# Optimization experiments

Hardware: AMD Instinct MI355X
Metric: run time of the kernel (lower is better)

Reference implementation:

```python
import jax, jax.numpy as jnp
import numpy as np

N, E = 50000, 800000
D_IN, D_HID, D_OUT = 128, 128, 64
BN_EPS = 1e-5
GEN_EPS = 1e-7


def _lin_init(k, fan_in, shape):
    lim = 1.0 / np.sqrt(fan_in)
    return jax.random.uniform(k, shape, minval=-lim, maxval=lim, dtype=jnp.float32)


def setup_inputs() -> dict:
    key = jax.random.key(0)
    ks = jax.random.split(key, 12)
    x = jax.random.normal(ks[0], (N, D_IN), dtype=jnp.float32)
    edge_index = jax.random.randint(ks[1], (2, E), 0, N, dtype=jnp.int64)
    return {
        "x": x,
        # GCNConv 0 and 1 (Glorot-ish uniform init like PyG Linear)
        "W0": _lin_init(ks[2], D_IN, (D_IN, D_HID)), "b0": jnp.zeros((D_HID,), jnp.float32),
        "g0": jnp.ones((D_HID,), jnp.float32), "beta0": jnp.zeros((D_HID,), jnp.float32),
        "W1": _lin_init(ks[3], D_HID, (D_HID, D_HID)), "b1": jnp.zeros((D_HID,), jnp.float32),
        "g1": jnp.ones((D_HID,), jnp.float32), "beta1": jnp.zeros((D_HID,), jnp.float32),
        # GENConv MLP: [D_HID] -> [2*D_HID] (BN+ReLU) -> [D_OUT]
        "Wg1": _lin_init(ks[4], D_HID, (D_HID, 2 * D_HID)), "bg1": jnp.zeros((2 * D_HID,), jnp.float32),
        "gg": jnp.ones((2 * D_HID,), jnp.float32), "betag": jnp.zeros((2 * D_HID,), jnp.float32),
        "Wg2": _lin_init(ks[5], 2 * D_HID, (2 * D_HID, D_OUT)), "bg2": jnp.zeros((D_OUT,), jnp.float32),
        "edge_index": edge_index,
    }


def _bn(h, gamma, beta):
    # BatchNorm1d, training-mode batch statistics (biased variance)
    mu = jnp.mean(h, axis=0)
    var = jnp.mean(jnp.square(h - mu), axis=0)
    return (h - mu) * jax.lax.rsqrt(var + BN_EPS) * gamma + beta


def _gcn_conv(x, W, b, src, dst, n):
    # GCNConv: D^-1/2 (A + I) D^-1/2 (x W) + b
    loop = jnp.arange(n, dtype=src.dtype)
    s = jnp.concatenate([src, loop])
    d = jnp.concatenate([dst, loop])
    deg = jax.ops.segment_sum(jnp.ones_like(s, dtype=x.dtype), d, num_segments=n)
    dinv = jax.lax.rsqrt(deg)  # deg >= 1 due to self-loops
    norm = dinv[s] * dinv[d]   # [E+N]
    h = x @ W                  # [N, D]
    agg = jax.ops.segment_sum(norm[:, None] * h[s], d, num_segments=n)
    return agg + b


def _gen_conv(x, W1, b1, g, beta, W2, b2, src, dst, n):
    # GENConv (defaults): msg = relu(x_j) + eps; per-channel softmax aggregation
    # (t=1); residual add of x_dst; then MLP [D, 2D (BN+ReLU), D_out].
    msg = jax.nn.relu(x[src]) + GEN_EPS            # [E, D]
    m = jax.ops.segment_max(msg, dst, num_segments=n)
    m = jnp.where(jnp.isfinite(m), m, 0.0)         # guard zero in-degree nodes
    ex = jnp.exp(msg - m[dst])                     # [E, D]
    denom = jax.ops.segment_sum(ex, dst, num_segments=n)
    num = jax.ops.segment_sum(ex * msg, dst, num_segments=n)
    agg = num / jnp.maximum(denom, 1e-16)          # [N, D]
    out = agg + x                                  # residual
    h = jax.nn.relu(_bn(out @ W1 + b1, g, beta))
    return h @ W2 + b2


def reference(x, W0, b0, g0, beta0, W1, b1, g1, beta1,
              Wg1, bg1, gg, betag, Wg2, bg2, edge_index):
    src, dst = edge_index[0], edge_index[1]
    n = x.shape[0]
    # layer 0: GCNConv -> BN -> ReLU (dropout is identity in eval)
    h = _gcn_conv(x, W0, b0, src, dst, n)
    h = jax.nn.relu(_bn(h, g0, beta0))
    # layer 1
    h = _gcn_conv(h, W1, b1, src, dst, n)
    h = jax.nn.relu(_bn(h, g1, beta1))
    # final GENConv + log-softmax over classes
    h = _gen_conv(h, Wg1, bg1, gg, betag, Wg2, bg2, src, dst, n)
    return jax.nn.log_softmax(h, axis=-1)
```

## Files before the change

kernel.cpp:

```cpp
#include <hip/hip_runtime.h>
#include <hip/hip_bf16.h>

#define DIN 128
#define DHID 128
#define DCLS 64
#define BN_EPS 1e-5f
#define GEN_EPS 1e-7f

typedef __attribute__((ext_vector_type(8))) short short8;
typedef __attribute__((ext_vector_type(4))) float f32x4;

static __device__ __forceinline__ float bf2f(unsigned short u) {
    union { float f; unsigned int i; } x; x.i = ((unsigned int)u) << 16; return x.f;
}
static __device__ __forceinline__ unsigned short f2bf(float f) {
    union { float f; unsigned int i; } x; x.f = f;
    unsigned int r = x.i + 0x7fffu + ((x.i >> 16) & 1u);
    return (unsigned short)(r >> 16);
}
static __device__ __forceinline__ float bflo(unsigned int u) {
    union { float f; unsigned int i; } x; x.i = u << 16; return x.f;
}
static __device__ __forceinline__ float bfhi(unsigned int u) {
    union { float f; unsigned int i; } x; x.i = u & 0xffff0000u; return x.f;
}
static __device__ __forceinline__ unsigned int packbf(float lo, float hi) {
    return ((unsigned int)f2bf(hi) << 16) | f2bf(lo);
}

__global__ void k_hist(const int* __restrict__ dst, int* __restrict__ counts, int E) {
    int e = blockIdx.x * 256 + threadIdx.x;
    if (e < E) atomicAdd(&counts[dst[e]], 1);
}

__global__ __launch_bounds__(256) void k_scan1(const int* __restrict__ counts,
        int* __restrict__ roff, int* __restrict__ bsum, int N) {
    __shared__ int ls[256];
    int t = threadIdx.x;
    int base = blockIdx.x * 1024 + t * 4;
    int c0 = 0, c1 = 0, c2 = 0, c3 = 0;
    if (base + 3 < N) {
        int4 v = *(const int4*)(counts + base);
        c0 = v.x; c1 = v.y; c2 = v.z; c3 = v.w;
    } else {
        if (base + 0 < N) c0 = counts[base + 0];
        if (base + 1 < N) c1 = counts[base + 1];
        if (base + 2 < N) c2 = counts[base + 2];
        if (base + 3 < N) c3 = counts[base + 3];
    }
    ls[t] = c0 + c1 + c2 + c3;
    __syncthreads();
    for (int off = 1; off < 256; off <<= 1) {
        int v = (t >= off) ? ls[t - off] : 0;
        __syncthreads();
        ls[t] += v;
        __syncthreads();
    }
    int r = (t == 0) ? 0 : ls[t - 1];
    if (base + 0 < N) { roff[base + 0] = r; r += c0; }
    if (base + 1 < N) { roff[base + 1] = r; r += c1; }
    if (base + 2 < N) { roff[base + 2] = r; r += c2; }
    if (base + 3 < N) { roff[base + 3] = r; }
    if (t == 255) bsum[blockIdx.x] = ls[255];
}

__global__ __launch_bounds__(1024) void k_scan2(int* __restrict__ bsum, int nblk) {
    __shared__ int ls[1024];
    int t = threadIdx.x;
    ls[t] = (t < nblk) ? bsum[t] : 0;
    __syncthreads();
    for (int off = 1; off < 1024; off <<= 1) {
        int v = (t >= off) ? ls[t - off] : 0;
        __syncthreads();
        ls[t] += v;
        __syncthreads();
    }
    if (t < nblk) bsum[t] = (t == 0) ? 0 : ls[t - 1];
}

__global__ void k_scan3(const int* __restrict__ counts, const int* __restrict__ bsum,
        int* __restrict__ roff, int* __restrict__ cursor, float* __restrict__ dinv,
        int N, int E) {
    int i = blockIdx.x * 256 + threadIdx.x;
    if (i < N) {
        int r = roff[i] + bsum[i >> 10];
        roff[i] = r; cursor[i] = r;
        dinv[i] = rsqrtf((float)(counts[i] + 1));
    }
    if (i == 0) roff[N] = E;
}

__global__ void k_fill(const int* __restrict__ src, const int* __restrict__ dst,
        int* __restrict__ cursor, int* __restrict__ srcs, int E) {
    int e = blockIdx.x * 256 + threadIdx.x;
    if (e < E) {
        int d = dst[e];
        int p = atomicAdd(&cursor[d], 1);
        srcs[p] = src[e];
    }
}

__global__ void k_wt(const float* __restrict__ W, unsigned short* __restrict__ Wt, int K, int Dout) {
    int i = blockIdx.x * 256 + threadIdx.x;
    if (i >= K * Dout) return;
    int n = i / K, k = i - n * K;
    Wt[i] = f2bf(W[(size_t)k * Dout + n]);
}

template<int K, bool ABF16, bool OBF16>
__global__ __launch_bounds__(256) void k_gemm(const void* __restrict__ Av,
        const unsigned short* __restrict__ Wt, const float* __restrict__ bias,
        const float* __restrict__ scale, const float* __restrict__ shift,
        const float* __restrict__ rowscale,
        void* __restrict__ Cv, int nrows, int Dout) {
    constexpr int KP = K + 8;
    __shared__ unsigned short sA[64 * KP];
    __shared__ unsigned short sW[64 * KP];
    const int tid = threadIdx.x;
    const int row0 = blockIdx.x * 64, col0 = blockIdx.y * 64;

#pragma unroll
    for (int it = 0; it < (64 * K) / (256 * 4); ++it) {
        int idx = (it * 256 + tid) * 4;
        int r = idx / K, c = idx % K;
        int gr = row0 + r;
        float v0 = 0.f, v1 = 0.f, v2 = 0.f, v3 = 0.f;
        if (gr < nrows) {
            if (ABF16) {
                ushort4 u = *(const ushort4*)((const unsigned short*)Av + (size_t)gr * K + c);
                v0 = bf2f(u.x); v1 = bf2f(u.y); v2 = bf2f(u.z); v3 = bf2f(u.w);
            } else {
                float4 f = *(const float4*)((const float*)Av + (size_t)gr * K + c);
                v0 = f.x; v1 = f.y; v2 = f.z; v3 = f.w;
            }
            if (scale) {
                v0 = fmaxf(v0 * scale[c + 0] + shift[c + 0], 0.f);
                v1 = fmaxf(v1 * scale[c + 1] + shift[c + 1], 0.f);
                v2 = fmaxf(v2 * scale[c + 2] + shift[c + 2], 0.f);
                v3 = fmaxf(v3 * scale[c + 3] + shift[c + 3], 0.f);
            }
        }
        ushort4 o; o.x = f2bf(v0); o.y = f2bf(v1); o.z = f2bf(v2); o.w = f2bf(v3);
        *(ushort4*)(&sA[r * KP + c]) = o;
    }
#pragma unroll
    for (int it = 0; it < (64 * K) / (256 * 8); ++it) {
        int idx = (it * 256 + tid) * 8;
        int r = idx / K, c = idx % K;
        uint4 u = *(const uint4*)(Wt + (size_t)(col0 + r) * K + c);
        *(uint4*)(&sW[r * KP + c]) = u;
    }
    __syncthreads();

    const int w = tid >> 6, lane = tid & 63;
    const int wr = (w >> 1) * 32, wc = (w & 1) * 32;
    const int lr = lane & 15, kg = (lane >> 4) * 8;
    f32x4 acc[2][2] = {};
#pragma unroll
    for (int kk = 0; kk < K; kk += 32) {
        short8 af[2], bfr[2];
#pragma unroll
        for (int mi = 0; mi < 2; mi++)
            af[mi] = *(const short8*)(&sA[(wr + mi * 16 + lr) * KP + kk + kg]);
#pragma unroll
        for (int ni = 0; ni < 2; ni++)
            bfr[ni] = *(const short8*)(&sW[(wc + ni * 16 + lr) * KP + kk + kg]);
#pragma unroll
        for (int mi = 0; mi < 2; mi++)
#pragma unroll
            for (int ni = 0; ni < 2; ni++)
                acc[mi][ni] = __builtin_amdgcn_mfma_f32_16x16x32_bf16(af[mi], bfr[ni], acc[mi][ni], 0, 0, 0);
    }
#pragma unroll
    for (int mi = 0; mi < 2; mi++) {
#pragma unroll
        for (int ni = 0; ni < 2; ni++) {
            int r = wr + mi * 16 + (lane >> 4) * 4;
            int cgl = col0 + wc + ni * 16 + (lane & 15);
            float bv = bias ? bias[cgl] : 0.f;
#pragma unroll
            for (int j = 0; j < 4; j++) {
                int gr = row0 + r + j;
                if (gr < nrows) {
                    float val = acc[mi][ni][j] + bv;
                    if (rowscale) val *= rowscale[gr];
                    if (OBF16) ((unsigned short*)Cv)[(size_t)gr * Dout + cgl] = f2bf(val);
                    else       ((float*)Cv)[(size_t)gr * Dout + cgl] = val;
                }
            }
        }
    }
}

__global__ __launch_bounds__(256) void k_gcn_agg(const unsigned short* __restrict__ p,
        const int* __restrict__ roff, const int* __restrict__ srcs,
        const float* __restrict__ dinv, const float* __restrict__ b,
        unsigned short* __restrict__ out,
        float* __restrict__ gsum, float* __restrict__ gsq, int N) {
    int nw = (gridDim.x * 256) >> 6;
    int wid = (blockIdx.x * 256 + threadIdx.x) >> 6;
    int lane = threadIdx.x & 63;
    int q = lane >> 4, l16 = lane & 15;
    int c = l16 * 8;
    float4 bl = *(const float4*)(b + c);
    float4 bh = *(const float4*)(b + c + 4);
    float bb[8] = {bl.x, bl.y, bl.z, bl.w, bh.x, bh.y, bh.z, bh.w};
    float ls[8] = {0,0,0,0,0,0,0,0};
    float lq[8] = {0,0,0,0,0,0,0,0};
    for (int d = wid; d < N; d += nw) {
        float a0=0.f,a1=0.f,a2=0.f,a3=0.f,a4=0.f,a5=0.f,a6=0.f,a7=0.f;
        int e0 = roff[d], e1 = roff[d + 1];
        for (int e = e0 + q; e < e1; e += 4) {
            int s = srcs[e];
            uint4 u = ((const uint4*)(p + (size_t)s * 128))[l16];
            a0 += bflo(u.x); a1 += bfhi(u.x);
            a2 += bflo(u.y); a3 += bfhi(u.y);
            a4 += bflo(u.z); a5 += bfhi(u.z);
            a6 += bflo(u.w); a7 += bfhi(u.w);
        }
        if (q == 0) {
            uint4 u = ((const uint4*)(p + (size_t)d * 128))[l16];
            a0 += bflo(u.x); a1 += bfhi(u.x);
            a2 += bflo(u.y); a3 += bfhi(u.y);
            a4 += bflo(u.z); a5 += bfhi(u.z);
            a6 += bflo(u.w); a7 += bfhi(u.w);
        }
        a0 += __shfl_xor(a0,16); a0 += __shfl_xor(a0,32);
        a1 += __shfl_xor(a1,16); a1 += __shfl_xor(a1,32);
        a2 += __shfl_xor(a2,16); a2 += __shfl_xor(a2,32);
        a3 += __shfl_xor(a3,16); a3 += __shfl_xor(a3,32);
        a4 += __shfl_xor(a4,16); a4 += __shfl_xor(a4,32);
        a5 += __shfl_xor(a5,16); a5 += __shfl_xor(a5,32);
        a6 += __shfl_xor(a6,16); a6 += __shfl_xor(a6,32);
        a7 += __shfl_xor(a7,16); a7 += __shfl_xor(a7,32);
        if (q == 0) {
            float dv = dinv[d];
            float r0 = dv*a0 + bb[0], r1 = dv*a1 + bb[1];
            float r2 = dv*a2 + bb[2], r3 = dv*a3 + bb[3];
            float r4 = dv*a4 + bb[4], r5 = dv*a5 + bb[5];
            float r6 = dv*a6 + bb[6], r7 = dv*a7 + bb[7];
            ls[0]+=r0; lq[0]+=r0*r0; ls[1]+=r1; lq[1]+=r1*r1;
            ls[2]+=r2; lq[2]+=r2*r2; ls[3]+=r3; lq[3]+=r3*r3;
            ls[4]+=r4; lq[4]+=r4*r4; ls[5]+=r5; lq[5]+=r5*r5;
            ls[6]+=r6; lq[6]+=r6*r6; ls[7]+=r7; lq[7]+=r7*r7;
            uint4 o;
            o.x = packbf(r0, r1); o.y = packbf(r2, r3);
            o.z = packbf(r4, r5); o.w = packbf(r6, r7);
            ((uint4*)(out + (size_t)d * 128))[l16] = o;
        }
    }
    __shared__ float sred[4][128];
    __shared__ float qred[4][128];
    int wv = threadIdx.x >> 6;
    if (q == 0) {
#pragma unroll
        for (int k = 0; k < 8; k++) { sred[wv][c + k] = ls[k]; qred[wv][c + k] = lq[k]; }
    }
    __syncthreads();
    int t = threadIdx.x;
    if (t < 128) {
        float s = sred[0][t] + sred[1][t] + sred[2][t] + sred[3][t];
        float qq = qred[0][t] + qred[1][t] + qred[2][t] + qred[3][t];
        atomicAdd(&gsum[t], s);
        atomicAdd(&gsq[t], qq);
    }
}

__global__ __launch_bounds__(256) void k_genpre(const unsigned short* __restrict__ t4,
        const float* __restrict__ scale, const float* __restrict__ shift,
        unsigned short* __restrict__ wt, int N) {
    int i = blockIdx.x * 256 + threadIdx.x;
    int node = i >> 4, l16 = i & 15;
    if (node >= N) return;
    int c = l16 * 8;
    float4 scl = *(const float4*)(scale + c);
    float4 sch = *(const float4*)(scale + c + 4);
    float4 shl = *(const float4*)(shift + c);
    float4 shh = *(const float4*)(shift + c + 4);
    float sc[8] = {scl.x, scl.y, scl.z, scl.w, sch.x, sch.y, sch.z, sch.w};
    float sh[8] = {shl.x, shl.y, shl.z, shl.w, shh.x, shh.y, shh.z, shh.w};
    uint4 u = ((const uint4*)(t4 + (size_t)node * 128))[l16];
    float v[8] = {bflo(u.x), bfhi(u.x), bflo(u.y), bfhi(u.y),
                  bflo(u.z), bfhi(u.z), bflo(u.w), bfhi(u.w)};
    float w[8], wm[8];
#pragma unroll
    for (int k = 0; k < 8; k++) {
        float m = fmaxf(v[k] * sc[k] + sh[k], 0.f) + GEN_EPS;
        m = fminf(m, 80.f);
        w[k] = __expf(m);
        wm[k] = w[k] * m;
    }
    uint4* row = (uint4*)(wt + (size_t)node * 256);
    uint4 ow, om;
    ow.x = packbf(w[0], w[1]); ow.y = packbf(w[2], w[3]);
    ow.z = packbf(w[4], w[5]); ow.w = packbf(w[6], w[7]);
    om.x = packbf(wm[0], wm[1]); om.y = packbf(wm[2], wm[3]);
    om.z = packbf(wm[4], wm[5]); om.w = packbf(wm[6], wm[7]);
    row[l16] = ow;
    row[16 + l16] = om;
}

__global__ __launch_bounds__(256) void k_gen_agg(const unsigned short* __restrict__ t4,
        const unsigned short* __restrict__ wt,
        const int* __restrict__ roff, const int* __restrict__ srcs,
        const float* __restrict__ scale, const float* __restrict__ shift,
        unsigned short* __restrict__ out, int N) {
    int nw = (gridDim.x * 256) >> 6;
    int wid = (blockIdx.x * 256 + threadIdx.x) >> 6;
    int lane = threadIdx.x & 63;
    int q = lane >> 4, l16 = lane & 15;
    int c = l16 * 8;
    for (int d = wid; d < N; d += nw) {
        float de[8] = {0,0,0,0,0,0,0,0};
        float nu[8] = {0,0,0,0,0,0,0,0};
        int e0 = roff[d], e1 = roff[d + 1];
        for (int e = e0 + q; e < e1; e += 4) {
            int s = srcs[e];
            const uint4* row = (const uint4*)(wt + (size_t)s * 256);
            uint4 uw = row[l16];
            uint4 um = row[16 + l16];
            de[0] += bflo(uw.x); de[1] += bfhi(uw.x);
            de[2] += bflo(uw.y); de[3] += bfhi(uw.y);
            de[4] += bflo(uw.z); de[5] += bfhi(uw.z);
            de[6] += bflo(uw.w); de[7] += bfhi(uw.w);
            nu[0] += bflo(um.x); nu[1] += bfhi(um.x);
            nu[2] += bflo(um.y); nu[3] += bfhi(um.y);
            nu[4] += bflo(um.z); nu[5] += bfhi(um.z);
            nu[6] += bflo(um.w); nu[7] += bfhi(um.w);
        }
#pragma unroll
        for (int k = 0; k < 8; k++) {
            de[k] += __shfl_xor(de[k],16); de[k] += __shfl_xor(de[k],32);
            nu[k] += __shfl_xor(nu[k],16); nu[k] += __shfl_xor(nu[k],32);
        }
        if (q == 0) {
            float4 scl = *(const float4*)(scale + c);
            float4 sch = *(const float4*)(scale + c + 4);
            float4 shl = *(const float4*)(shift + c);
            float4 shh = *(const float4*)(shift + c + 4);
            float sc[8] = {scl.x, scl.y, scl.z, scl.w, sch.x, sch.y, sch.z, sch.w};
            float sh[8] = {shl.x, shl.y, shl.z, shl.w, shh.x, shh.y, shh.z, shh.w};
            uint4 u = ((const uint4*)(t4 + (size_t)d * 128))[l16];
            float v[8] = {bflo(u.x), bfhi(u.x), bflo(u.y), bfhi(u.y),
                          bflo(u.z), bfhi(u.z), bflo(u.w), bfhi(u.w)};
            float r[8];
            bool has = (e1 > e0);
#pragma unroll
            for (int k = 0; k < 8; k++) {
                float h2 = fmaxf(v[k] * sc[k] + sh[k], 0.f);
                float a = has ? nu[k] / de[k] : 0.f;
                r[k] = a + h2;
            }
            uint4 o;
            o.x = packbf(r[0], r[1]); o.y = packbf(r[2], r[3]);
            o.z = packbf(r[4], r[5]); o.w = packbf(r[6], r[7]);
            ((uint4*)(out + (size_t)d * 128))[l16] = o;
        }
    }
}

template<int D>
__global__ __launch_bounds__(256) void k_stats(const unsigned short* __restrict__ h,
        float* __restrict__ gsum, float* __restrict__ gsq, int N) {
    constexpr int HC = D / 2, TPC = 256 / HC;
    int t = threadIdx.x;
    int cp = t % HC, slot = t / HC;
    int c = cp * 2;
    float s0 = 0.f, s1 = 0.f, q0 = 0.f, q1 = 0.f;
    for (int node = blockIdx.x * TPC + slot; node < N; node += gridDim.x * TPC) {
        ushort2 u = *(const ushort2*)(h + (size_t)node * D + c);
        float v0 = bf2f(u.x), v1 = bf2f(u.y);
        s0 += v0; s1 += v1; q0 += v0 * v0; q1 += v1 * v1;
    }
    __shared__ float red[256 * 4];
    red[t * 4] = s0; red[t * 4 + 1] = s1; red[t * 4 + 2] = q0; red[t * 4 + 3] = q1;
    __syncthreads();
    if (slot == 0) {
        for (int k2 = 1; k2 < TPC; k2++) {
            int o = (t + k2 * HC) * 4;
            s0 += red[o]; s1 += red[o + 1]; q0 += red[o + 2]; q1 += red[o + 3];
        }
        atomicAdd(&gsum[c], s0); atomicAdd(&gsum[c + 1], s1);
        atomicAdd(&gsq[c], q0); atomicAdd(&gsq[c + 1], q1);
    }
}

__global__ void k_fin(const float* __restrict__ sum, const float* __restrict__ sq,
        const float* __restrict__ g, const float* __restrict__ beta,
        float* __restrict__ scale, float* __restrict__ shift, int D, float invN) {
    int c = threadIdx.x;
    if (c < D) {
        float mu = sum[c] * invN;
        float var = sq[c] * invN - mu * mu;
        float s = g[c] * rsqrtf(var + BN_EPS);
        scale[c] = s;
        shift[c] = beta[c] - mu * s;
    }
}

__global__ __launch_bounds__(256) void k_head(float* __restrict__ out, int N) {
    int wid = blockIdx.x * 4 + (threadIdx.x >> 6);
    int lane = threadIdx.x & 63;
    if (wid >= N) return;
    float v = out[(size_t)wid * 64 + lane];
    float m = v;
    for (int o = 32; o; o >>= 1) m = fmaxf(m, __shfl_xor(m, o));
    float e = __expf(v - m);
    float s = e;
    for (int o = 32; o; o >>= 1) s += __shfl_xor(s, o);
    out[(size_t)wid * 64 + lane] = v - m - __logf(s);
}

extern "C" void kernel_launch(void* const* d_in, const int* in_sizes, int n_in,
                              void* d_out, int out_size, void* d_ws, size_t ws_size,
                              hipStream_t stream) {
    const float* x   = (const float*)d_in[0];
    const float* W0  = (const float*)d_in[1];
    const float* b0  = (const float*)d_in[2];
    const float* g0  = (const float*)d_in[3];
    const float* be0 = (const float*)d_in[4];
    const float* W1  = (const float*)d_in[5];
    const float* b1  = (const float*)d_in[6];
    const float* g1  = (const float*)d_in[7];
    const float* be1 = (const float*)d_in[8];
    const float* Wg1 = (const float*)d_in[9];
    const float* bg1 = (const float*)d_in[10];
    const float* gg  = (const float*)d_in[11];
    const float* beg = (const float*)d_in[12];
    const float* Wg2 = (const float*)d_in[13];
    const float* bg2 = (const float*)d_in[14];
    const int*   ei  = (const int*)d_in[15];

    const int N = in_sizes[0] / DIN;
    const int E = in_sizes[15] / 2;
    const int* src = ei;
    const int* dst = ei + E;

    char* ws = (char*)d_ws;
    size_t off = 0;
    auto alloc = [&](size_t b) { size_t o = off; off = (off + b + 255) & ~(size_t)255; return o; };
    size_t o_counts = alloc((size_t)N * 4);
    size_t o_stats  = alloc(1024 * 4);
    size_t o_cursor = alloc((size_t)N * 4);
    size_t o_roff   = alloc(((size_t)N + 1) * 4);
    size_t o_srcs   = alloc((size_t)E * 4);
    size_t o_dinv   = alloc((size_t)N * 4);
    size_t o_bsum   = alloc(1024 * 4);
    size_t o_ss     = alloc(1024 * 4);
    size_t o_w0t    = alloc(128 * 128 * 2);
    size_t o_w1t    = alloc(128 * 128 * 2);
    size_t o_wg1t   = alloc(256 * 128 * 2);
    size_t o_wg2t   = alloc(64 * 256 * 2);
    size_t o_xa     = alloc((size_t)N * 128 * 2);
    size_t o_xb     = alloc((size_t)N * 128 * 2);
    size_t o_c      = alloc((size_t)N * 256 * 2);
    (void)ws_size; (void)n_in; (void)out_size;

    int* counts = (int*)(ws + o_counts);
    float* stats = (float*)(ws + o_stats);
    int* cursor = (int*)(ws + o_cursor);
    int* roff = (int*)(ws + o_roff);
    int* srcs = (int*)(ws + o_srcs);
    float* dinv = (float*)(ws + o_dinv);
    int* bsum = (int*)(ws + o_bsum);
    float* ssz = (float*)(ws + o_ss);
    unsigned short* w0t  = (unsigned short*)(ws + o_w0t);
    unsigned short* w1t  = (unsigned short*)(ws + o_w1t);
    unsigned short* wg1t = (unsigned short*)(ws + o_wg1t);
    unsigned short* wg2t = (unsigned short*)(ws + o_wg2t);
    unsigned short* xa = (unsigned short*)(ws + o_xa);
    unsigned short* xb = (unsigned short*)(ws + o_xb);
    unsigned short* cb = (unsigned short*)(ws + o_c);
    unsigned short* wtab = cb;

    float* sum0 = stats;       float* sq0 = stats + 128;
    float* sum1 = stats + 256; float* sq1 = stats + 384;
    float* sumg = stats + 512; float* sqg = stats + 768;
    float* scale0 = ssz;       float* shift0 = ssz + 128;
    float* scale1 = ssz + 256; float* shift1 = ssz + 384;
    float* scaleg = ssz + 512; float* shiftg = ssz + 768;

    hipMemsetAsync(ws + o_counts, 0, o_cursor - o_counts, stream);

    int egrid = (E + 255) / 256;
    int nblk = (N + 1023) / 1024;
    k_hist<<<egrid, 256, 0, stream>>>(dst, counts, E);
    k_scan1<<<nblk, 256, 0, stream>>>(counts, roff, bsum, N);
    k_scan2<<<1, 1024, 0, stream>>>(bsum, nblk);
    k_scan3<<<(N + 255) / 256, 256, 0, stream>>>(counts, bsum, roff, cursor, dinv, N, E);
    k_fill<<<egrid, 256, 0, stream>>>(src, dst, cursor, srcs, E);

    k_wt<<<(128 * 128 + 255) / 256, 256, 0, stream>>>(W0, w0t, 128, 128);
    k_wt<<<(128 * 128 + 255) / 256, 256, 0, stream>>>(W1, w1t, 128, 128);
    k_wt<<<(128 * 256 + 255) / 256, 256, 0, stream>>>(Wg1, wg1t, 128, 256);
    k_wt<<<(256 * 64 + 255) / 256, 256, 0, stream>>>(Wg2, wg2t, 256, 64);

    int rb = (N + 63) / 64;
    const float invN = 1.f / (float)N;

    k_gemm<128, false, true><<<dim3(rb, 2), 256, 0, stream>>>(x, w0t, nullptr, nullptr, nullptr, dinv, xa, N, 128);
    k_gcn_agg<<<2048, 256, 0, stream>>>(xa, roff, srcs, dinv, b0, xb, sum0, sq0, N);
    k_fin<<<1, 256, 0, stream>>>(sum0, sq0, g0, be0, scale0, shift0, 128, invN);

    k_gemm<128, true, true><<<dim3(rb, 2), 256, 0, stream>>>(xb, w1t, nullptr, scale0, shift0, dinv, xa, N, 128);
    k_gcn_agg<<<2048, 256, 0, stream>>>(xa, roff, srcs, dinv, b1, xb, sum1, sq1, N);
    k_fin<<<1, 256, 0, stream>>>(sum1, sq1, g1, be1, scale1, shift1, 128, invN);

    k_genpre<<<(N * 16 + 255) / 256, 256, 0, stream>>>(xb, scale1, shift1, wtab, N);
    k_gen_agg<<<2048, 256, 0, stream>>>(xb, wtab, roff, srcs, scale1, shift1, xa, N);

    k_gemm<128, true, true><<<dim3(rb, 4), 256, 0, stream>>>(xa, wg1t, bg1, nullptr, nullptr, nullptr, cb, N, 256);
    k_stats<256><<<1024, 256, 0, stream>>>(cb, sumg, sqg, N);
    k_fin<<<1, 256, 0, stream>>>(sumg, sqg, gg, beg, scaleg, shiftg, 256, invN);
    k_gemm<256, true, false><<<dim3(rb, 1), 256, 0, stream>>>(cb, wg2t, bg2, scaleg, shiftg, nullptr, d_out, N, 64);

    k_head<<<(N + 3) / 4, 256, 0, stream>>>((float*)d_out, N);
}
```

Before: 499.9 us.

## Slice node features into 16-channel tables so each XCD aggregates one slice

GEMM outputs and GEN precomputed weights are written in a channel-sliced layout (8 slices of 16 channels, each contiguous over nodes). The GCN and GEN aggregation kernels assign each block one slice via blockIdx&7 and gather only that slice. The per-slice tables are small enough to stay resident in a per-XCD L2, which is meant to cut random-gather traffic to HBM. In exchange, the edge lists and offsets are re-read once per slice, and more lanes are spent per edge on narrower loads.

After: 617.2 us. +23.5%, slower.

```diff
diff --git a/kernel.cpp b/kernel.cpp
--- a/kernel.cpp
+++ b/kernel.cpp
@@ -107,7 +107,7 @@
     Wt[i] = f2bf(W[(size_t)k * Dout + n]);
 }
 
-template<int K, bool ABF16, bool OBF16>
+template<int K, bool ABF16, bool OBF16, bool SLICED>
 __global__ __launch_bounds__(256) void k_gemm(const void* __restrict__ Av,
         const unsigned short* __restrict__ Wt, const float* __restrict__ bias,
         const float* __restrict__ scale, const float* __restrict__ shift,
@@ -184,8 +184,14 @@
                 if (gr < nrows) {
                     float val = acc[mi][ni][j] + bv;
                     if (rowscale) val *= rowscale[gr];
-                    if (OBF16) ((unsigned short*)Cv)[(size_t)gr * Dout + cgl] = f2bf(val);
-                    else       ((float*)Cv)[(size_t)gr * Dout + cgl] = val;
+                    if (OBF16) {
+                        size_t addr = SLICED
+                            ? ((size_t)(cgl >> 4) * nrows + gr) * 16 + (cgl & 15)
+                            : (size_t)gr * Dout + cgl;
+                        ((unsigned short*)Cv)[addr] = f2bf(val);
+                    } else {
+                        ((float*)Cv)[(size_t)gr * Dout + cgl] = val;
+                    }
                 }
             }
         }
@@ -197,72 +203,60 @@
         const float* __restrict__ dinv, const float* __restrict__ b,
         unsigned short* __restrict__ out,
         float* __restrict__ gsum, float* __restrict__ gsq, int N) {
-    int nw = (gridDim.x * 256) >> 6;
-    int wid = (blockIdx.x * 256 + threadIdx.x) >> 6;
+    int slice = blockIdx.x & 7;
+    int c0 = slice * 16;
+    const unsigned short* ps = p + (size_t)slice * N * 16;
+    int wv = threadIdx.x >> 6;
     int lane = threadIdx.x & 63;
-    int q = lane >> 4, l16 = lane & 15;
-    int c = l16 * 8;
-    float4 bl = *(const float4*)(b + c);
-    float4 bh = *(const float4*)(b + c + 4);
-    float bb[8] = {bl.x, bl.y, bl.z, bl.w, bh.x, bh.y, bh.z, bh.w};
-    float ls[8] = {0,0,0,0,0,0,0,0};
-    float lq[8] = {0,0,0,0,0,0,0,0};
+    int grp = lane >> 2, l4 = lane & 3;
+    int wid = (blockIdx.x >> 3) * 4 + wv;
+    int nw = (gridDim.x >> 3) * 4;
+    float4 bv4 = *(const float4*)(b + c0 + l4 * 4);
+    float ls0 = 0.f, ls1 = 0.f, ls2 = 0.f, ls3 = 0.f;
+    float lq0 = 0.f, lq1 = 0.f, lq2 = 0.f, lq3 = 0.f;
     for (int d = wid; d < N; d += nw) {
-        float a0=0.f,a1=0.f,a2=0.f,a3=0.f,a4=0.f,a5=0.f,a6=0.f,a7=0.f;
+        float a0 = 0.f, a1 = 0.f, a2 = 0.f, a3 = 0.f;
         int e0 = roff[d], e1 = roff[d + 1];
-        for (int e = e0 + q; e < e1; e += 4) {
+        for (int e = e0 + grp; e < e1; e += 16) {
             int s = srcs[e];
-            uint4 u = ((const uint4*)(p + (size_t)s * 128))[l16];
+            uint2 u = *(const uint2*)(ps + (size_t)s * 16 + l4 * 4);
             a0 += bflo(u.x); a1 += bfhi(u.x);
             a2 += bflo(u.y); a3 += bfhi(u.y);
-            a4 += bflo(u.z); a5 += bfhi(u.z);
-            a6 += bflo(u.w); a7 += bfhi(u.w);
-        }
-        if (q == 0) {
-            uint4 u = ((const uint4*)(p + (size_t)d * 128))[l16];
+        }
+        if (grp == 0) {
+            uint2 u = *(const uint2*)(ps + (size_t)d * 16 + l4 * 4);
             a0 += bflo(u.x); a1 += bfhi(u.x);
             a2 += bflo(u.y); a3 += bfhi(u.y);
-            a4 += bflo(u.z); a5 += bfhi(u.z);
-            a6 += bflo(u.w); a7 += bfhi(u.w);
-        }
-        a0 += __shfl_xor(a0,16); a0 += __shfl_xor(a0,32);
-        a1 += __shfl_xor(a1,16); a1 += __shfl_xor(a1,32);
-        a2 += __shfl_xor(a2,16); a2 += __shfl_xor(a2,32);
-        a3 += __shfl_xor(a3,16); a3 += __shfl_xor(a3,32);
-        a4 += __shfl_xor(a4,16); a4 += __shfl_xor(a4,32);
-        a5 += __shfl_xor(a5,16); a5 += __shfl_xor(a5,32);
-        a6 += __shfl_xor(a6,16); a6 += __shfl_xor(a6,32);
-        a7 += __shfl_xor(a7,16); a7 += __shfl_xor(a7,32);
-        if (q == 0) {
+        }
+        for (int off = 4; off < 64; off <<= 1) {
+            a0 += __shfl_xor(a0, off); a1 += __shfl_xor(a1, off);
+            a2 += __shfl_xor(a2, off); a3 += __shfl_xor(a3, off);
+        }
+        if (grp == 0) {
             float dv = dinv[d];
-            float r0 = dv*a0 + bb[0], r1 = dv*a1 + bb[1];
-            float r2 = dv*a2 + bb[2], r3 = dv*a3 + bb[3];
-            float r4 = dv*a4 + bb[4], r5 = dv*a5 + bb[5];
-            float r6 = dv*a6 + bb[6], r7 = dv*a7 + bb[7];
-            ls[0]+=r0; lq[0]+=r0*r0; ls[1]+=r1; lq[1]+=r1*r1;
-            ls[2]+=r2; lq[2]+=r2*r2; ls[3]+=r3; lq[3]+=r3*r3;
-            ls[4]+=r4; lq[4]+=r4*r4; ls[5]+=r5; lq[5]+=r5*r5;
-            ls[6]+=r6; lq[6]+=r6*r6; ls[7]+=r7; lq[7]+=r7*r7;
-            uint4 o;
-            o.x = packbf(r0, r1); o.y = packbf(r2, r3);
-            o.z = packbf(r4, r5); o.w = packbf(r6, r7);
-            ((uint4*)(out + (size_t)d * 128))[l16] = o;
-        }
-    }
-    __shared__ float sred[4][128];
-    __shared__ float qred[4][128];
-    int wv = threadIdx.x >> 6;
-    if (q == 0) {
-#pragma unroll
-        for (int k = 0; k < 8; k++) { sred[wv][c + k] = ls[k]; qred[wv][c + k] = lq[k]; }
+            float r0 = dv * a0 + bv4.x, r1 = dv * a1 + bv4.y;
+            float r2 = dv * a2 + bv4.z, r3 = dv * a3 + bv4.w;
+            ls0 += r0; lq0 += r0 * r0; ls1 += r1; lq1 += r1 * r1;
+            ls2 += r2; lq2 += r2 * r2; ls3 += r3; lq3 += r3 * r3;
+            uint2 o; o.x = packbf(r0, r1); o.y = packbf(r2, r3);
+            *(uint2*)(out + (size_t)d * 128 + c0 + l4 * 4) = o;
+        }
+    }
+    __shared__ float sred[4][16];
+    __shared__ float qred[4][16];
+    if (grp == 0) {
+        sred[wv][l4 * 4 + 0] = ls0; sred[wv][l4 * 4 + 1] = ls1;
+        sred[wv][l4 * 4 + 2] = ls2; sred[wv][l4 * 4 + 3] = ls3;
+        qred[wv][l4 * 4 + 0] = lq0; qred[wv][l4 * 4 + 1] = lq1;
+        qred[wv][l4 * 4 + 2] = lq2; qred[wv][l4 * 4 + 3] = lq3;
     }
     __syncthreads();
     int t = threadIdx.x;
-    if (t < 128) {
+    if (t < 16) {
         float s = sred[0][t] + sred[1][t] + sred[2][t] + sred[3][t];
         float qq = qred[0][t] + qred[1][t] + qred[2][t] + qred[3][t];
-        atomicAdd(&gsum[t], s);
-        atomicAdd(&gsq[t], qq);
+        atomicAdd(&gsum[c0 + t], s);
+        atomicAdd(&gsq[c0 + t], qq);
     }
 }
 
@@ -290,14 +284,15 @@
         w[k] = __expf(m);
         wm[k] = w[k] * m;
     }
-    uint4* row = (uint4*)(wt + (size_t)node * 256);
+    int slice = l16 >> 1, half = l16 & 1;
+    unsigned short* base = wt + (size_t)slice * N * 32 + (size_t)node * 32 + half * 8;
     uint4 ow, om;
     ow.x = packbf(w[0], w[1]); ow.y = packbf(w[2], w[3]);
     ow.z = packbf(w[4], w[5]); ow.w = packbf(w[6], w[7]);
     om.x = packbf(wm[0], wm[1]); om.y = packbf(wm[2], wm[3]);
     om.z = packbf(wm[4], wm[5]); om.w = packbf(wm[6], wm[7]);
-    row[l16] = ow;
-    row[16 + l16] = om;
+    *(uint4*)base = ow;
+    *(uint4*)(base + 16) = om;
 }
 
 __global__ __launch_bounds__(256) void k_gen_agg(const unsigned short* __restrict__ t4,
@@ -305,56 +300,45 @@
         const int* __restrict__ roff, const int* __restrict__ srcs,
         const float* __restrict__ scale, const float* __restrict__ shift,
         unsigned short* __restrict__ out, int N) {
-    int nw = (gridDim.x * 256) >> 6;
-    int wid = (blockIdx.x * 256 + threadIdx.x) >> 6;
+    int slice = blockIdx.x & 7;
+    int c0 = slice * 16;
+    const unsigned short* wts = wt + (size_t)slice * N * 32;
+    int wv = threadIdx.x >> 6;
     int lane = threadIdx.x & 63;
-    int q = lane >> 4, l16 = lane & 15;
-    int c = l16 * 8;
+    int grp = lane >> 3, l8 = lane & 7;
+    int wid = (blockIdx.x >> 3) * 4 + wv;
+    int nw = (gridDim.x >> 3) * 4;
     for (int d = wid; d < N; d += nw) {
-        float de[8] = {0,0,0,0,0,0,0,0};
-        float nu[8] = {0,0,0,0,0,0,0,0};
+        float a0 = 0.f, a1 = 0.f, a2 = 0.f, a3 = 0.f;
         int e0 = roff[d], e1 = roff[d + 1];
-        for (int e = e0 + q; e < e1; e += 4) {
+        for (int e = e0 + grp; e < e1; e += 8) {
             int s = srcs[e];
-            const uint4* row = (const uint4*)(wt + (size_t)s * 256);
-            uint4 uw = row[l16];
-            uint4 um = row[16 + l16];
-            de[0] += bflo(uw.x); de[1] += bfhi(uw.x);
-            de[2] += bflo(uw.y); de[3] += bfhi(uw.y);
-            de[4] += bflo(uw.z); de[5] += bfhi(uw.z);
-            de[6] += bflo(uw.w); de[7] += bfhi(uw.w);
-            nu[0] += bflo(um.x); nu[1] += bfhi(um.x);
-            nu[2] += bflo(um.y); nu[3] += bfhi(um.y);
-            nu[4] += bflo(um.z); nu[5] += bfhi(um.z);
-            nu[6] += bflo(um.w); nu[7] += bfhi(um.w);
-        }
-#pragma unroll
-        for (int k = 0; k < 8; k++) {
-            de[k] += __shfl_xor(de[k],16); de[k] += __shfl_xor(de[k],32);
-            nu[k] += __shfl_xor(nu[k],16); nu[k] += __shfl_xor(nu[k],32);
-        }
-        if (q == 0) {
-            float4 scl = *(const float4*)(scale + c);
-            float4 sch = *(const float4*)(scale + c + 4);
-            float4 shl = *(const float4*)(shift + c);
-            float4 shh = *(const float4*)(shift + c + 4);
-            float sc[8] = {scl.x, scl.y, scl.z, scl.w, sch.x, sch.y, sch.z, sch.w};
-            float sh[8] = {shl.x, shl.y, shl.z, shl.w, shh.x, shh.y, shh.z, shh.w};
-            uint4 u = ((const uint4*)(t4 + (size_t)d * 128))[l16];
-            float v[8] = {bflo(u.x), bfhi(u.x), bflo(u.y), bfhi(u.y),
-                          bflo(u.z), bfhi(u.z), bflo(u.w), bfhi(u.w)};
-            float r[8];
+            uint2 u = *(const uint2*)(wts + (size_t)s * 32 + l8 * 4);
+            a0 += bflo(u.x); a1 += bfhi(u.x);
+            a2 += bflo(u.y); a3 += bfhi(u.y);
+        }
+        for (int off = 8; off < 64; off <<= 1) {
+            a0 += __shfl_xor(a0, off); a1 += __shfl_xor(a1, off);
+            a2 += __shfl_xor(a2, off); a3 += __shfl_xor(a3, off);
+        }
+        float n0 = __shfl_xor(a0, 4), n1 = __shfl_xor(a1, 4);
+        float n2 = __shfl_xor(a2, 4), n3 = __shfl_xor(a3, 4);
+        if (grp == 0 && l8 < 4) {
             bool has = (e1 > e0);
-#pragma unroll
-            for (int k = 0; k < 8; k++) {
-                float h2 = fmaxf(v[k] * sc[k] + sh[k], 0.f);
-                float a = has ? nu[k] / de[k] : 0.f;
-                r[k] = a + h2;
-            }
-            uint4 o;
-            o.x = packbf(r[0], r[1]); o.y = packbf(r[2], r[3]);
-            o.z = packbf(r[4], r[5]); o.w = packbf(r[6], r[7]);
-            ((uint4*)(out + (size_t)d * 128))[l16] = o;
+            float i0 = has ? n0 / a0 : 0.f;
+            float i1 = has ? n1 / a1 : 0.f;
+            float i2 = has ? n2 / a2 : 0.f;
+            float i3 = has ? n3 / a3 : 0.f;
+            int cc = c0 + l8 * 4;
+            float4 sc4 = *(const float4*)(scale + cc);
+            float4 sh4 = *(const float4*)(shift + cc);
+            uint2 u = *(const uint2*)(t4 + (size_t)d * 128 + cc);
+            float r0 = i0 + fmaxf(bflo(u.x) * sc4.x + sh4.x, 0.f);
+            float r1 = i1 + fmaxf(bfhi(u.x) * sc4.y + sh4.y, 0.f);
+            float r2 = i2 + fmaxf(bflo(u.y) * sc4.z + sh4.z, 0.f);
+            float r3 = i3 + fmaxf(bfhi(u.y) * sc4.w + sh4.w, 0.f);
+            uint2 o; o.x = packbf(r0, r1); o.y = packbf(r2, r3);
+            *(uint2*)(out + (size_t)d * 128 + cc) = o;
         }
     }
 }
@@ -498,21 +482,21 @@
     int rb = (N + 63) / 64;
     const float invN = 1.f / (float)N;
 
-    k_gemm<128, false, true><<<dim3(rb, 2), 256, 0, stream>>>(x, w0t, nullptr, nullptr, nullptr, dinv, xa, N, 128);
+    k_gemm<128, false, true, true><<<dim3(rb, 2), 256, 0, stream>>>(x, w0t, nullptr, nullptr, nullptr, dinv, xa, N, 128);
     k_gcn_agg<<<2048, 256, 0, stream>>>(xa, roff, srcs, dinv, b0, xb, sum0, sq0, N);
     k_fin<<<1, 256, 0, stream>>>(sum0, sq0, g0, be0, scale0, shift0, 128, invN);
 
-    k_gemm<128, true, true><<<dim3(rb, 2), 256, 0, stream>>>(xb, w1t, nullptr, scale0, shift0, dinv, xa, N, 128);
+    k_gemm<128, true, true, true><<<dim3(rb, 2), 256, 0, stream>>>(xb, w1t, nullptr, scale0, shift0, dinv, xa, N, 128);
     k_gcn_agg<<<2048, 256, 0, stream>>>(xa, roff, srcs, dinv, b1, xb, sum1, sq1, N);
     k_fin<<<1, 256, 0, stream>>>(sum1, sq1, g1, be1, scale1, shift1, 128, invN);
 
     k_genpre<<<(N * 16 + 255) / 256, 256, 0, stream>>>(xb, scale1, shift1, wtab, N);
     k_gen_agg<<<2048, 256, 0, stream>>>(xb, wtab, roff, srcs, scale1, shift1, xa, N);
 
-    k_gemm<128, true, true><<<dim3(rb, 4), 256, 0, stream>>>(xa, wg1t, bg1, nullptr, nullptr, nullptr, cb, N, 256);
+    k_gemm<128, true, true, false><<<dim3(rb, 4), 256, 0, stream>>>(xa, wg1t, bg1, nullptr, nullptr, nullptr, cb, N, 256);
     k_stats<256><<<1024, 256, 0, stream>>>(cb, sumg, sqg, N);
     k_fin<<<1, 256, 0, stream>>>(sumg, sqg, gg, beg, scaleg, shiftg, 256, invN);
-    k_gemm<256, true, false><<<dim3(rb, 1), 256, 0, stream>>>(cb, wg2t, bg2, scaleg, shiftg, nullptr, d_out, N, 64);
+    k_gemm<256, true, false, false><<<dim3(rb, 1), 256, 0, stream>>>(cb, wg2t, bg2, scaleg, shiftg, nullptr, d_out, N, 64);
 
     k_head<<<(N + 3) / 4, 256, 0, stream>>>((float*)d_out, N);
 }
```

## Fuse BN statistics and log-softmax head into GEMM epilogues, widen column tiles

Applied to the files above, without the earlier changes.

The GEMM kernel is generalised to a configurable column tile, so each block covers 128 columns and the A tile is read and converted fewer times. The K loop is chunked at 128 so the shared-memory footprint stays bounded. BatchNorm sum and sum-of-squares are now accumulated in the GENConv first-GEMM epilogue through shared-memory then global atomics, which replaces the separate stats kernel and its re-read of the 256-wide activation. Log-softmax is fused into the final GEMM through a padded shared tile, which removes the separate head kernel and a round-trip of the output. The cost is more registers per thread and fewer blocks in the grid, which may lower occupancy.

New measurement: 477.7 us. 1.05x faster.

```diff
diff --git a/kernel.cpp b/kernel.cpp
--- a/kernel.cpp
+++ b/kernel.cpp
@@ -107,76 +107,95 @@
     Wt[i] = f2bf(W[(size_t)k * Dout + n]);
 }
 
-template<int K, bool ABF16, bool OBF16>
+template<int K, int CTILE, bool ABF16, bool OBF16, bool STATS, bool HEAD>
 __global__ __launch_bounds__(256) void k_gemm(const void* __restrict__ Av,
         const unsigned short* __restrict__ Wt, const float* __restrict__ bias,
         const float* __restrict__ scale, const float* __restrict__ shift,
         const float* __restrict__ rowscale,
-        void* __restrict__ Cv, int nrows, int Dout) {
-    constexpr int KP = K + 8;
-    __shared__ unsigned short sA[64 * KP];
-    __shared__ unsigned short sW[64 * KP];
+        void* __restrict__ Cv, float* __restrict__ gsum, float* __restrict__ gsq,
+        int nrows, int Dout) {
+    constexpr int KP = 136;
+    constexpr int NF = CTILE / 32;
+    __shared__ unsigned short smem[(64 + CTILE) * KP];
+    unsigned short* sA = smem;
+    unsigned short* sW = smem + 64 * KP;
     const int tid = threadIdx.x;
-    const int row0 = blockIdx.x * 64, col0 = blockIdx.y * 64;
-
-#pragma unroll
-    for (int it = 0; it < (64 * K) / (256 * 4); ++it) {
-        int idx = (it * 256 + tid) * 4;
-        int r = idx / K, c = idx % K;
-        int gr = row0 + r;
-        float v0 = 0.f, v1 = 0.f, v2 = 0.f, v3 = 0.f;
-        if (gr < nrows) {
-            if (ABF16) {
-                ushort4 u = *(const ushort4*)((const unsigned short*)Av + (size_t)gr * K + c);
-                v0 = bf2f(u.x); v1 = bf2f(u.y); v2 = bf2f(u.z); v3 = bf2f(u.w);
-            } else {
-                float4 f = *(const float4*)((const float*)Av + (size_t)gr * K + c);
-                v0 = f.x; v1 = f.y; v2 = f.z; v3 = f.w;
+    const int row0 = blockIdx.x * 64, col0 = blockIdx.y * CTILE;
+
+    const int w = tid >> 6, lane = tid & 63;
+    const int wr = (w >> 1) * 32, wc = (w & 1) * (CTILE / 2);
+    const int lr = lane & 15, kg = (lane >> 4) * 8;
+    f32x4 acc[2][NF] = {};
+
+    for (int kh = 0; kh < K; kh += 128) {
+#pragma unroll
+        for (int it = 0; it < 8; ++it) {
+            int idx = (it * 256 + tid) * 4;
+            int r = idx >> 7, c = idx & 127;
+            int gr = row0 + r;
+            float v0 = 0.f, v1 = 0.f, v2 = 0.f, v3 = 0.f;
+            if (gr < nrows) {
+                if (ABF16) {
+                    ushort4 u = *(const ushort4*)((const unsigned short*)Av + (size_t)gr * K + kh + c);
+                    v0 = bf2f(u.x); v1 = bf2f(u.y); v2 = bf2f(u.z); v3 = bf2f(u.w);
+                } else {
+                    float4 f = *(const float4*)((const float*)Av + (size_t)gr * K + kh + c);
+                    v0 = f.x; v1 = f.y; v2 = f.z; v3 = f.w;
+                }
+                if (scale) {
+                    int cc = kh + c;
+                    v0 = fmaxf(v0 * scale[cc + 0] + shift[cc + 0], 0.f);
+                    v1 = fmaxf(v1 * scale[cc + 1] + shift[cc + 1], 0.f);
+                    v2 = fmaxf(v2 * scale[cc + 2] + shift[cc + 2], 0.f);
+                    v3 = fmaxf(v3 * scale[cc + 3] + shift[cc + 3], 0.f);
+                }
             }
-            if (scale) {
-                v0 = fmaxf(v0 * scale[c + 0] + shift[c + 0], 0.f);
-                v1 = fmaxf(v1 * scale[c + 1] + shift[c + 1], 0.f);
-                v2 = fmaxf(v2 * scale[c + 2] + shift[c + 2], 0.f);
-                v3 = fmaxf(v3 * scale[c + 3] + shift[c + 3], 0.f);
-            }
-        }
-        ushort4 o; o.x = f2bf(v0); o.y = f2bf(v1); o.z = f2bf(v2); o.w = f2bf(v3);
-        *(ushort4*)(&sA[r * KP + c]) = o;
-    }
-#pragma unroll
-    for (int it = 0; it < (64 * K) / (256 * 8); ++it) {
-        int idx = (it * 256 + tid) * 8;
-        int r = idx / K, c = idx % K;
-        uint4 u = *(const uint4*)(Wt + (size_t)(col0 + r) * K + c);
-        *(uint4*)(&sW[r * KP + c]) = u;
-    }
-    __syncthreads();
-
-    const int w = tid >> 6, lane = tid & 63;
-    const int wr = (w >> 1) * 32, wc = (w & 1) * 32;
-    const int lr = lane & 15, kg = (lane >> 4) * 8;
-    f32x4 acc[2][2] = {};
-#pragma unroll
-    for (int kk = 0; kk < K; kk += 32) {
-        short8 af[2], bfr[2];
-#pragma unroll
-        for (int mi = 0; mi < 2; mi++)
-            af[mi] = *(const short8*)(&sA[(wr + mi * 16 + lr) * KP + kk + kg]);
-#pragma unroll
-        for (int ni = 0; ni < 2; ni++)
-            bfr[ni] = *(const short8*)(&sW[(wc + ni * 16 + lr) * KP + kk + kg]);
-#pragma unroll
-        for (int mi = 0; mi < 2; mi++)
-#pragma unroll
-            for (int ni = 0; ni < 2; ni++)
-                acc[mi][ni] = __builtin_amdgcn_mfma_f32_16x16x32_bf16(af[mi], bfr[ni], acc[mi][ni], 0, 0, 0);
-    }
+            ushort4 o; o.x = f2bf(v0); o.y = f2bf(v1); o.z = f2bf(v2); o.w = f2bf(v3);
+            *(ushort4*)(&sA[r * KP + c]) = o;
+        }
+#pragma unroll
+        for (int it = 0; it < (CTILE * 128) / (256 * 8); ++it) {
+            int idx = (it * 256 + tid) * 8;
+            int r = idx >> 7, c = idx & 127;
+            uint4 u = *(const uint4*)(Wt + (size_t)(col0 + r) * K + kh + c);
+            *(uint4*)(&sW[r * KP + c]) = u;
+        }
+        __syncthreads();
+#pragma unroll
+        for (int kk = 0; kk < 128; kk += 32) {
+            short8 af[2], bfr[NF];
+#pragma unroll
+            for (int mi = 0; mi < 2; mi++)
+                af[mi] = *(const short8*)(&sA[(wr + mi * 16 + lr) * KP + kk + kg]);
+#pragma unroll
+            for (int ni = 0; ni < NF; ni++)
+                bfr[ni] = *(const short8*)(&sW[(wc + ni * 16 + lr) * KP + kk + kg]);
+#pragma unroll
+            for (int mi = 0; mi < 2; mi++)
+#pragma unroll
+                for (int ni = 0; ni < NF; ni++)
+                    acc[mi][ni] = __builtin_amdgcn_mfma_f32_16x16x32_bf16(af[mi], bfr[ni], acc[mi][ni], 0, 0, 0);
+        }
+        __syncthreads();
+    }
+
+    float* fs = (float*)smem;
+    if (STATS) {
+        if (tid < 2 * CTILE) fs[tid] = 0.f;
+        __syncthreads();
+    }
+
+    float stat_s[NF], stat_q[NF];
+#pragma unroll
+    for (int ni = 0; ni < NF; ni++) { stat_s[ni] = 0.f; stat_q[ni] = 0.f; }
+
 #pragma unroll
     for (int mi = 0; mi < 2; mi++) {
 #pragma unroll
-        for (int ni = 0; ni < 2; ni++) {
+        for (int ni = 0; ni < NF; ni++) {
             int r = wr + mi * 16 + (lane >> 4) * 4;
-            int cgl = col0 + wc + ni * 16 + (lane & 15);
+            int cloc = wc + ni * 16 + (lane & 15);
+            int cgl = col0 + cloc;
             float bv = bias ? bias[cgl] : 0.f;
 #pragma unroll
             for (int j = 0; j < 4; j++) {
@@ -184,13 +203,54 @@
                 if (gr < nrows) {
                     float val = acc[mi][ni][j] + bv;
                     if (rowscale) val *= rowscale[gr];
-                    if (OBF16) ((unsigned short*)Cv)[(size_t)gr * Dout + cgl] = f2bf(val);
-                    else       ((float*)Cv)[(size_t)gr * Dout + cgl] = val;
+                    if (STATS) { stat_s[ni] += val; stat_q[ni] += val * val; }
+                    if (HEAD) {
+                        fs[(r + j) * 65 + cloc] = val;
+                    } else if (OBF16) {
+                        ((unsigned short*)Cv)[(size_t)gr * Dout + cgl] = f2bf(val);
+                    } else {
+                        ((float*)Cv)[(size_t)gr * Dout + cgl] = val;
+                    }
+                } else if (HEAD) {
+                    fs[(r + j) * 65 + cloc] = 0.f;
                 }
             }
         }
     }
-}
+
+    if (STATS) {
+#pragma unroll
+        for (int ni = 0; ni < NF; ni++) {
+            int cloc = wc + ni * 16 + (lane & 15);
+            atomicAdd(&fs[cloc], stat_s[ni]);
+            atomicAdd(&fs[CTILE + cloc], stat_q[ni]);
+        }
+        __syncthreads();
+        if (tid < CTILE) {
+            atomicAdd(&gsum[col0 + tid], fs[tid]);
+            atomicAdd(&gsq[col0 + tid], fs[CTILE + tid]);
+        }
+    }
+
+    if (HEAD) {
+        __syncthreads();
+        for (int rr = 0; rr < 16; rr++) {
+            int row = w * 16 + rr;
+            int gr = row0 + row;
+            if (gr >= nrows) break;
+            float v = fs[row * 65 + lane];
+            float m = v;
+            for (int o = 32; o; o >>= 1) m = fmaxf(m, __shfl_xor(m, o));
+            float e = __expf(v - m);
+            float s = e;
+            for (int o = 32; o; o >>= 1) s += __shfl_xor(s, o);
+            ((float*)Cv)[(size_t)gr * 64 + lane] = v - m - __logf(s);
+        }
+    }
+}
+
+#define ACC8(u) { a0 += bflo(u.x); a1 += bfhi(u.x); a2 += bflo(u.y); a3 += bfhi(u.y); \
+                  a4 += bflo(u.z); a5 += bfhi(u.z); a6 += bflo(u.w); a7 += bfhi(u.w); }
 
 __global__ __launch_bounds__(256) void k_gcn_agg(const unsigned short* __restrict__ p,
         const int* __restrict__ roff, const int* __restrict__ srcs,
@@ -213,17 +273,11 @@
         for (int e = e0 + q; e < e1; e += 4) {
             int s = srcs[e];
             uint4 u = ((const uint4*)(p + (size_t)s * 128))[l16];
-            a0 += bflo(u.x); a1 += bfhi(u.x);
-            a2 += bflo(u.y); a3 += bfhi(u.y);
-            a4 += bflo(u.z); a5 += bfhi(u.z);
-            a6 += bflo(u.w); a7 += bfhi(u.w);
+            ACC8(u);
         }
         if (q == 0) {
             uint4 u = ((const uint4*)(p + (size_t)d * 128))[l16];
-            a0 += bflo(u.x); a1 += bfhi(u.x);
-            a2 += bflo(u.y); a3 += bfhi(u.y);
-            a4 += bflo(u.z); a5 += bfhi(u.z);
-            a6 += bflo(u.w); a7 += bfhi(u.w);
+            ACC8(u);
         }
         a0 += __shfl_xor(a0,16); a0 += __shfl_xor(a0,32);
         a1 += __shfl_xor(a1,16); a1 += __shfl_xor(a1,32);
@@ -359,32 +413,6 @@
     }
 }
 
-template<int D>
-__global__ __launch_bounds__(256) void k_stats(const unsigned short* __restrict__ h,
-        float* __restrict__ gsum, float* __restrict__ gsq, int N) {
-    constexpr int HC = D / 2, TPC = 256 / HC;
-    int t = threadIdx.x;
-    int cp = t % HC, slot = t / HC;
-    int c = cp * 2;
-    float s0 = 0.f, s1 = 0.f, q0 = 0.f, q1 = 0.f;
-    for (int node = blockIdx.x * TPC + slot; node < N; node += gridDim.x * TPC) {
-        ushort2 u = *(const ushort2*)(h + (size_t)node * D + c);
-        float v0 = bf2f(u.x), v1 = bf2f(u.y);
-        s0 += v0; s1 += v1; q0 += v0 * v0; q1 += v1 * v1;
-    }
-    __shared__ float red[256 * 4];
-    red[t * 4] = s0; red[t * 4 + 1] = s1; red[t * 4 + 2] = q0; red[t * 4 + 3] = q1;
-    __syncthreads();
-    if (slot == 0) {
-        for (int k2 = 1; k2 < TPC; k2++) {
-            int o = (t + k2 * HC) * 4;
-            s0 += red[o]; s1 += red[o + 1]; q0 += red[o + 2]; q1 += red[o + 3];
-        }
-        atomicAdd(&gsum[c], s0); atomicAdd(&gsum[c + 1], s1);
-        atomicAdd(&gsq[c], q0); atomicAdd(&gsq[c + 1], q1);
-    }
-}
-
 __global__ void k_fin(const float* __restrict__ sum, const float* __restrict__ sq,
         const float* __restrict__ g, const float* __restrict__ beta,
         float* __restrict__ scale, float* __restrict__ shift, int D, float invN) {
@@ -396,19 +424,6 @@
         scale[c] = s;
         shift[c] = beta[c] - mu * s;
     }
-}
-
-__global__ __launch_bounds__(256) void k_head(float* __restrict__ out, int N) {
-    int wid = blockIdx.x * 4 + (threadIdx.x >> 6);
-    int lane = threadIdx.x & 63;
-    if (wid >= N) return;
-    float v = out[(size_t)wid * 64 + lane];
-    float m = v;
-    for (int o = 32; o; o >>= 1) m = fmaxf(m, __shfl_xor(m, o));
-    float e = __expf(v - m);
-    float s = e;
-    for (int o = 32; o; o >>= 1) s += __shfl_xor(s, o);
-    out[(size_t)wid * 64 + lane] = v - m - __logf(s);
 }
 
 extern "C" void kernel_launch(void* const* d_in, const int* in_sizes, int n_in,
@@ -498,21 +513,23 @@
     int rb = (N + 63) / 64;
     const float invN = 1.f / (float)N;
 
-    k_gemm<128, false, true><<<dim3(rb, 2), 256, 0, stream>>>(x, w0t, nullptr, nullptr, nullptr, dinv, xa, N, 128);
+    k_gemm<128, 128, false, true, false, false><<<dim3(rb, 1), 256, 0, stream>>>(
+        x, w0t, nullptr, nullptr, nullptr, dinv, xa, nullptr, nullptr, N, 128);
     k_gcn_agg<<<2048, 256, 0, stream>>>(xa, roff, srcs, dinv, b0, xb, sum0, sq0, N);
     k_fin<<<1, 256, 0, stream>>>(sum0, sq0, g0, be0, scale0, shift0, 128, invN);
 
-    k_gemm<128, true, true><<<dim3(rb, 2), 256, 0, stream>>>(xb, w1t, nullptr, scale0, shift0, dinv, xa, N, 128);
+    k_gemm<128, 128, true, true, false, false><<<dim3(rb, 1), 256, 0, stream>>>(
+        xb, w1t, nullptr, scale0, shift0, dinv, xa, nullptr, nullptr, N, 128);
     k_gcn_agg<<<2048, 256, 0, stream>>>(xa, roff, srcs, dinv, b1, xb, sum1, sq1, N);
     k_fin<<<1, 256, 0, stream>>>(sum1, sq1, g1, be1, scale1, shift1, 128, invN);
 
     k_genpre<<<(N * 16 + 255) / 256, 256, 0, stream>>>(xb, scale1, shift1, wtab, N);
     k_gen_agg<<<2048, 256, 0, stream>>>(xb, wtab, roff, srcs, scale1, shift1, xa, N);
 
-    k_gemm<128, true, true><<<dim3(rb, 4), 256, 0, stream>>>(xa, wg1t, bg1, nullptr, nullptr, nullptr, cb, N, 256);
-    k_stats<256><<<1024, 256, 0, stream>>>(cb, sumg, sqg, N);
+    k_gemm<128, 128, true, true, true, false><<<dim3(rb, 2), 256, 0, stream>>>(
+        xa, wg1t, bg1, nullptr, nullptr, nullptr, cb, sumg, sqg, N, 256);
     k_fin<<<1, 256, 0, stream>>>(sumg, sqg, gg, beg, scaleg, shiftg, 256, invN);
-    k_gemm<256, true, false><<<dim3(rb, 1), 256, 0, stream>>>(cb, wg2t, bg2, scaleg, shiftg, nullptr, d_out, N, 64);
-
-    k_head<<<(N + 3) / 4, 256, 0, stream>>>((float*)d_out, N);
-}
+
+    k_gemm<256, 64, true, false, false, true><<<dim3(rb, 1), 256, 0, stream>>>(
+        cb, wg2t, bg2, scaleg, shiftg, nullptr, d_out, nullptr, nullptr, N, 64);
+}
```
